# Performance work log

Measured on AMD Instinct MI355X. Metric: run time of the kernel, lower is better.

## Reference

```python
import jax, jax.numpy as jnp
import numpy as np

N_NODES = 50000
N_EDGES = 800000
IN_F = 128
OUT_F = 64
ALPHA = 0.2  # LeakyReLU negative slope


def setup_inputs() -> dict:
    key = jax.random.key(0)
    k_h, k_e, k_w, k_b, k_a = jax.random.split(key, 5)
    h = jax.random.normal(k_h, (N_NODES, IN_F), dtype=jnp.float32)
    adj = jax.random.randint(k_e, (2, N_EDGES), 0, N_NODES, dtype=jnp.int64)
    # Linear(in_features, out_features): weight [out, in], bias [out]
    W_w = jax.random.normal(k_w, (OUT_F, IN_F), dtype=jnp.float32) * (1.0 / np.sqrt(IN_F))
    W_b = jax.random.normal(k_b, (OUT_F,), dtype=jnp.float32) * 0.01
    a = jax.random.normal(k_a, (1, 2 * OUT_F), dtype=jnp.float32) * (1.0 / np.sqrt(2 * OUT_F))
    return {"h": h, "adj": adj, "W_w": W_w, "W_b": W_b, "a": a}


def reference(h, adj, W_w, W_b, a):
    N = h.shape[0]
    F_out = W_w.shape[0]
    inv_sqrt_f = 1.0 / float(np.sqrt(F_out))

    data = h @ W_w.T + W_b                      # [N, F_out]
    src, dst = adj[0], adj[1]

    # a @ [data[src] || data[dst]]^T  == (data @ a_src)[src] + (data @ a_dst)[dst]
    a_src, a_dst = a[0, :F_out], a[0, F_out:]
    score = (data @ a_src)[src] + (data @ a_dst)[dst]       # [E]
    edge_e = jnp.exp(jax.nn.leaky_relu(score, ALPHA) * inv_sqrt_f)

    # sparse rowsum over source rows (duplicate edges sum, matching COO semantics)
    rowsum = jax.ops.segment_sum(edge_e, src, num_segments=N)  # [N]
    row_zero = rowsum == 0.0
    rowsum = jnp.where(row_zero, 1.0, rowsum)

    # sparse mm: sum_e edge_e * data[dst] into row src; zero rows get a unit self-loop
    h_prime = jax.ops.segment_sum(edge_e[:, None] * data[dst], src, num_segments=N)
    h_prime = h_prime + row_zero[:, None].astype(data.dtype) * data
    return h_prime / rowsum[:, None]
```

## Files before the change

kernel.cpp:

```cpp
#include <hip/hip_runtime.h>
#include <math.h>

#define IN_F 128
#define OUT_F 64
#define ALPHA 0.2f
#define INV_SQRT_F 0.125f
#define CAP 64
#define BINSH 7
#define BINSZ 128
#define CAPB 4096
#define HS 136

typedef _Float16 h8  __attribute__((ext_vector_type(8)));
typedef float    f4  __attribute__((ext_vector_type(4)));

__device__ __forceinline__ float edge_w(float sc) {
    float lr = sc > 0.f ? sc : ALPHA * sc;
    return __expf(lr * INV_SQRT_F);
}

__device__ __forceinline__ h8 cvt8(float4 a, float4 b) {
    h8 r;
    r[0] = (_Float16)a.x; r[1] = (_Float16)a.y;
    r[2] = (_Float16)a.z; r[3] = (_Float16)a.w;
    r[4] = (_Float16)b.x; r[5] = (_Float16)b.y;
    r[6] = (_Float16)b.z; r[7] = (_Float16)b.w;
    return r;
}

__global__ __launch_bounds__(256, 4) void k_p1(
    const float* __restrict__ h, const float* __restrict__ W,
    const float* __restrict__ b, const float* __restrict__ a,
    const int* __restrict__ src, const int* __restrict__ dst,
    int* __restrict__ gcur, unsigned* __restrict__ pk,
    _Float16* __restrict__ data_h,
    float* __restrict__ s_src, float* __restrict__ s_dst,
    int n_nodes, int n_edges, int g_p1)
{
    __shared__ _Float16 wsh[OUT_F * HS];
    __shared__ int hist[512];
    __shared__ int off[512];
    const int tid = threadIdx.x;

    if ((int)blockIdx.x < g_p1) {
        const int nbins = (n_nodes + BINSZ - 1) >> BINSH;
        const int e0 = (int)blockIdx.x * 4096 + tid * 16;

        for (int i = tid; i < nbins; i += 256) hist[i] = 0;
        __syncthreads();

        int s[16], d[16];
        const bool full = (e0 + 16 <= n_edges);
        if (full) {
            #pragma unroll
            for (int c = 0; c < 4; ++c) {
                int4 s4 = *(const int4*)&src[e0 + c * 4];
                int4 d4 = *(const int4*)&dst[e0 + c * 4];
                s[c*4+0] = s4.x; s[c*4+1] = s4.y; s[c*4+2] = s4.z; s[c*4+3] = s4.w;
                d[c*4+0] = d4.x; d[c*4+1] = d4.y; d[c*4+2] = d4.z; d[c*4+3] = d4.w;
            }
            #pragma unroll
            for (int i = 0; i < 16; ++i)
                atomicAdd(&hist[s[i] >> BINSH], 1);
        } else {
            #pragma unroll
            for (int i = 0; i < 16; ++i) {
                int e = e0 + i;
                s[i] = (e < n_edges) ? src[e] : -1;
                d[i] = (e < n_edges) ? dst[e] : 0;
                if (s[i] >= 0) atomicAdd(&hist[s[i] >> BINSH], 1);
            }
        }
        __syncthreads();

        for (int i = tid; i < nbins; i += 256) {
            int c = hist[i];
            off[i] = (c > 0) ? atomicAdd(&gcur[i], c) : 0;
            hist[i] = 0;
        }
        __syncthreads();

        #pragma unroll
        for (int i = 0; i < 16; ++i) {
            if (s[i] < 0) continue;
            int bin = s[i] >> BINSH;
            int r = atomicAdd(&hist[bin], 1);
            int p = off[bin] + r;
            if (p < CAPB)
                pk[(size_t)bin * CAPB + p] =
                    ((unsigned)(s[i] & (BINSZ - 1)) << 16) | (unsigned)d[i];
        }
        return;
    }

    const int node0 = ((int)blockIdx.x - g_p1) * 64;

    const int wv  = tid >> 6;
    const int lane = tid & 63;
    const int q   = lane >> 4;
    const int col = lane & 15;
    const int r0  = wv * 16;

    const int arow = min(node0 + r0 + col, n_nodes - 1);
    const float* __restrict__ hrow = h + (size_t)arow * IN_F;

    float4 ha[4], hb[4];
    #pragma unroll
    for (int kk = 0; kk < 4; ++kk) {
        const int ko = kk * 32 + q * 8;
        ha[kk] = *(const float4*)&hrow[ko];
        hb[kk] = *(const float4*)&hrow[ko + 4];
    }
    float bb[4], as_[4], ad_[4];
    #pragma unroll
    for (int ct = 0; ct < 4; ++ct) {
        bb[ct]  = b[ct * 16 + col];
        as_[ct] = a[ct * 16 + col];
        ad_[ct] = a[OUT_F + ct * 16 + col];
    }

    for (int i = tid * 8; i < OUT_F * IN_F; i += 2048) {
        int f = i >> 7, k = i & 127;
        float4 va = *(const float4*)&W[i];
        float4 vb = *(const float4*)&W[i + 4];
        *(h8*)&wsh[f * HS + k] = cvt8(va, vb);
    }
    __syncthreads();

    f4 acc[4] = {{0.f,0.f,0.f,0.f},{0.f,0.f,0.f,0.f},
                 {0.f,0.f,0.f,0.f},{0.f,0.f,0.f,0.f}};
    #pragma unroll
    for (int kk = 0; kk < 4; ++kk) {
        const int ko = kk * 32 + q * 8;
        h8 av = cvt8(ha[kk], hb[kk]);
        #pragma unroll
        for (int ct = 0; ct < 4; ++ct) {
            h8 bv = *(const h8*)&wsh[(ct * 16 + col) * HS + ko];
            acc[ct] = __builtin_amdgcn_mfma_f32_16x16x32_f16(av, bv, acc[ct], 0, 0, 0);
        }
    }

    #pragma unroll
    for (int reg = 0; reg < 4; ++reg) {
        int n = node0 + r0 + q * 4 + reg;
        float vv[4], ps = 0.f, pd = 0.f;
        #pragma unroll
        for (int ct = 0; ct < 4; ++ct) {
            float v = acc[ct][reg] + bb[ct];
            vv[ct] = v;
            ps = fmaf(v, as_[ct], ps);
            pd = fmaf(v, ad_[ct], pd);
        }
        #pragma unroll
        for (int m = 1; m <= 8; m <<= 1) {
            ps += __shfl_xor(ps, m, 64);
            pd += __shfl_xor(pd, m, 64);
        }
        if (n < n_nodes) {
            size_t base = (size_t)n * OUT_F + col;
            #pragma unroll
            for (int ct = 0; ct < 4; ++ct)
                data_h[base + ct * 16] = (_Float16)vv[ct];
            if (col == 0) { s_src[n] = ps; s_dst[n] = pd; }
        }
    }
}

__global__ __launch_bounds__(512) void k_bin(
    const unsigned* __restrict__ pk, const int* __restrict__ gcur,
    const float* __restrict__ s_src, const float* __restrict__ s_dst,
    const _Float16* __restrict__ data_h, float* __restrict__ out, int n_nodes)
{
    __shared__ uint2 edl[64 * CAP];
    __shared__ int   lcnt[64];
    __shared__ float ssl[64];
    const int bin  = (int)blockIdx.x >> 1;
    const int half = (int)blockIdx.x & 1;
    const int tid  = threadIdx.x;
    const int nbase = bin * BINSZ + half * 64;

    if (tid < 64) {
        lcnt[tid] = 0;
        int n = nbase + tid;
        ssl[tid] = (n < n_nodes) ? s_src[n] : 0.f;
    }
    __syncthreads();

    const int ecnt = min(gcur[bin], CAPB);
    for (int i = tid; i < ecnt; i += 512) {
        unsigned v = pk[(size_t)bin * CAPB + i];
        int sl = (int)(v >> 16);
        if ((sl >> 6) == half) {
            int s63 = sl & 63;
            int d = (int)(v & 0xffffu);
            float w = edge_w(ssl[s63] + s_dst[d]);
            int r = atomicAdd(&lcnt[s63], 1);
            if (r < CAP) {
                uint2 e; e.x = (unsigned)d; e.y = __float_as_uint(w);
                edl[s63 * CAP + r] = e;
            }
        }
    }
    __syncthreads();

    const int wv = tid >> 6, lane = tid & 63;
    const int g  = lane >> 3;
    const int fl = lane & 7;

    #pragma unroll 1
    for (int ni = 0; ni < 8; ++ni) {
        const int nl = wv * 8 + ni;
        const int n = nbase + nl;
        if (n >= n_nodes) break;
        const int cn = min(lcnt[nl], CAP);
        const int bbase = nl * CAP;

        float ac[8] = {0.f,0.f,0.f,0.f,0.f,0.f,0.f,0.f};
        float rs = 0.f;
        int t = 0;
        for (; t + 16 <= cn; t += 16) {
            uint2 e0 = edl[bbase + t + g];
            uint2 e1 = edl[bbase + t + 8 + g];
            float w0 = __uint_as_float(e0.y);
            float w1 = __uint_as_float(e1.y);
            h8 x0 = *(const h8*)&data_h[(size_t)e0.x * OUT_F + 8 * fl];
            h8 x1 = *(const h8*)&data_h[(size_t)e1.x * OUT_F + 8 * fl];
            #pragma unroll
            for (int i = 0; i < 8; ++i) ac[i] = fmaf(w0, (float)x0[i], ac[i]);
            #pragma unroll
            for (int i = 0; i < 8; ++i) ac[i] = fmaf(w1, (float)x1[i], ac[i]);
            rs += w0 + w1;
        }
        for (; t + 8 <= cn; t += 8) {
            uint2 e0 = edl[bbase + t + g];
            float w0 = __uint_as_float(e0.y);
            h8 x0 = *(const h8*)&data_h[(size_t)e0.x * OUT_F + 8 * fl];
            #pragma unroll
            for (int i = 0; i < 8; ++i) ac[i] = fmaf(w0, (float)x0[i], ac[i]);
            rs += w0;
        }
        const int rem = cn - t;
        if (g < rem) {
            uint2 e0 = edl[bbase + t + g];
            float w0 = __uint_as_float(e0.y);
            h8 x0 = *(const h8*)&data_h[(size_t)e0.x * OUT_F + 8 * fl];
            #pragma unroll
            for (int i = 0; i < 8; ++i) ac[i] = fmaf(w0, (float)x0[i], ac[i]);
            rs += w0;
        }
        #pragma unroll
        for (int m = 8; m <= 32; m <<= 1) {
            #pragma unroll
            for (int i = 0; i < 8; ++i) ac[i] += __shfl_xor(ac[i], m, 64);
            rs += __shfl_xor(rs, m, 64);
        }

        if (g == 0) {
            size_t o = (size_t)n * OUT_F + 8 * fl;
            f4 r0, r1;
            if (rs == 0.f) {
                h8 xv = *(const h8*)&data_h[o];
                r0[0] = (float)xv[0]; r0[1] = (float)xv[1];
                r0[2] = (float)xv[2]; r0[3] = (float)xv[3];
                r1[0] = (float)xv[4]; r1[1] = (float)xv[5];
                r1[2] = (float)xv[6]; r1[3] = (float)xv[7];
            } else {
                float inv = 1.f / rs;
                r0[0] = ac[0] * inv; r0[1] = ac[1] * inv;
                r0[2] = ac[2] * inv; r0[3] = ac[3] * inv;
                r1[0] = ac[4] * inv; r1[1] = ac[5] * inv;
                r1[2] = ac[6] * inv; r1[3] = ac[7] * inv;
            }
            __builtin_nontemporal_store(r0, (f4*)&out[o]);
            __builtin_nontemporal_store(r1, (f4*)&out[o + 4]);
        }
    }
}

extern "C" void kernel_launch(void* const* d_in, const int* in_sizes, int n_in,
                              void* d_out, int out_size, void* d_ws, size_t ws_size,
                              hipStream_t stream)
{
    const float* h   = (const float*)d_in[0];
    const int*   adj = (const int*)  d_in[1];
    const float* W   = (const float*)d_in[2];
    const float* b   = (const float*)d_in[3];
    const float* a   = (const float*)d_in[4];
    float* out = (float*)d_out;

    const int n_nodes = in_sizes[0] / IN_F;
    const int n_edges = in_sizes[1] / 2;
    const int* src = adj;
    const int* dst = adj + n_edges;
    const int nbins = (n_nodes + BINSZ - 1) >> BINSH;

    char* p = (char*)d_ws;
    _Float16*       data_h = (_Float16*)p;       p += (size_t)n_nodes * OUT_F * 2;
    unsigned*       pk     = (unsigned*)p;       p += (size_t)nbins * CAPB * 4;
    float*          s_src  = (float*)p;          p += (size_t)n_nodes * 4;
    float*          s_dst  = (float*)p;          p += (size_t)n_nodes * 4;
    int*            gcur   = (int*)p;            p += (size_t)nbins * 4;

    (void)hipMemsetAsync(gcur, 0, (size_t)nbins * sizeof(int), stream);

    const int g_p1  = (n_edges + 4095) / 4096;
    const int g_lin = (n_nodes + 63) / 64;
    k_p1<<<g_p1 + g_lin, 256, 0, stream>>>(
        h, W, b, a, src, dst, gcur, pk, data_h, s_src, s_dst,
        n_nodes, n_edges, g_p1);

    k_bin<<<nbins * 2, 512, 0, stream>>>(
        pk, gcur, s_src, s_dst, data_h, out, n_nodes);
}
```

Measured before the change: 125.8 us.

## Assign one node per 8-lane group and rotate LDS edge slots

The aggregation phase drops the per-node loop where a whole wave split each node's edges across 8 lane groups and then reduced them with shuffles. Now each 8-lane group handles one node alone, walking its edges serially with 4-way unrolled gathers, so the cross-group shuffle reduction disappears. Edge slots in LDS are rotated by node index so that groups reading different nodes at the same step hit different banks. This trades fewer shuffles and less idle time on short lists for load imbalance between groups whose nodes have different degrees, and for a serial dependency chain per group.

```diff
diff --git a/kernel.cpp b/kernel.cpp
--- a/kernel.cpp
+++ b/kernel.cpp
@@ -197,7 +197,7 @@
             int r = atomicAdd(&lcnt[s63], 1);
             if (r < CAP) {
                 uint2 e; e.x = (unsigned)d; e.y = __float_as_uint(w);
-                edl[s63 * CAP + r] = e;
+                edl[s63 * CAP + ((r + 2 * (s63 & 7)) & (CAP - 1))] = e;
             }
         }
     }
@@ -206,74 +206,65 @@
     const int wv = tid >> 6, lane = tid & 63;
     const int g  = lane >> 3;
     const int fl = lane & 7;
-
-    #pragma unroll 1
-    for (int ni = 0; ni < 8; ++ni) {
-        const int nl = wv * 8 + ni;
-        const int n = nbase + nl;
-        if (n >= n_nodes) break;
-        const int cn = min(lcnt[nl], CAP);
-        const int bbase = nl * CAP;
-
-        float ac[8] = {0.f,0.f,0.f,0.f,0.f,0.f,0.f,0.f};
-        float rs = 0.f;
-        int t = 0;
-        for (; t + 16 <= cn; t += 16) {
-            uint2 e0 = edl[bbase + t + g];
-            uint2 e1 = edl[bbase + t + 8 + g];
-            float w0 = __uint_as_float(e0.y);
-            float w1 = __uint_as_float(e1.y);
-            h8 x0 = *(const h8*)&data_h[(size_t)e0.x * OUT_F + 8 * fl];
-            h8 x1 = *(const h8*)&data_h[(size_t)e1.x * OUT_F + 8 * fl];
-            #pragma unroll
-            for (int i = 0; i < 8; ++i) ac[i] = fmaf(w0, (float)x0[i], ac[i]);
-            #pragma unroll
-            for (int i = 0; i < 8; ++i) ac[i] = fmaf(w1, (float)x1[i], ac[i]);
-            rs += w0 + w1;
-        }
-        for (; t + 8 <= cn; t += 8) {
-            uint2 e0 = edl[bbase + t + g];
-            float w0 = __uint_as_float(e0.y);
-            h8 x0 = *(const h8*)&data_h[(size_t)e0.x * OUT_F + 8 * fl];
-            #pragma unroll
-            for (int i = 0; i < 8; ++i) ac[i] = fmaf(w0, (float)x0[i], ac[i]);
-            rs += w0;
-        }
-        const int rem = cn - t;
-        if (g < rem) {
-            uint2 e0 = edl[bbase + t + g];
-            float w0 = __uint_as_float(e0.y);
-            h8 x0 = *(const h8*)&data_h[(size_t)e0.x * OUT_F + 8 * fl];
-            #pragma unroll
-            for (int i = 0; i < 8; ++i) ac[i] = fmaf(w0, (float)x0[i], ac[i]);
-            rs += w0;
-        }
-        #pragma unroll
-        for (int m = 8; m <= 32; m <<= 1) {
-            #pragma unroll
-            for (int i = 0; i < 8; ++i) ac[i] += __shfl_xor(ac[i], m, 64);
-            rs += __shfl_xor(rs, m, 64);
-        }
-
-        if (g == 0) {
-            size_t o = (size_t)n * OUT_F + 8 * fl;
-            f4 r0, r1;
-            if (rs == 0.f) {
-                h8 xv = *(const h8*)&data_h[o];
-                r0[0] = (float)xv[0]; r0[1] = (float)xv[1];
-                r0[2] = (float)xv[2]; r0[3] = (float)xv[3];
-                r1[0] = (float)xv[4]; r1[1] = (float)xv[5];
-                r1[2] = (float)xv[6]; r1[3] = (float)xv[7];
-            } else {
-                float inv = 1.f / rs;
-                r0[0] = ac[0] * inv; r0[1] = ac[1] * inv;
-                r0[2] = ac[2] * inv; r0[3] = ac[3] * inv;
-                r1[0] = ac[4] * inv; r1[1] = ac[5] * inv;
-                r1[2] = ac[6] * inv; r1[3] = ac[7] * inv;
-            }
-            __builtin_nontemporal_store(r0, (f4*)&out[o]);
-            __builtin_nontemporal_store(r1, (f4*)&out[o + 4]);
-        }
+    const int nl = wv * 8 + g;
+    const int n  = nbase + nl;
+    const int rot = 2 * (nl & 7);
+    const int cn = (n < n_nodes) ? min(lcnt[nl], CAP) : 0;
+    const int bbase = nl * CAP;
+
+    float ac[8] = {0.f,0.f,0.f,0.f,0.f,0.f,0.f,0.f};
+    float rs = 0.f;
+    int t = 0;
+    for (; t + 4 <= cn; t += 4) {
+        uint2 e0 = edl[bbase + ((t + 0 + rot) & (CAP - 1))];
+        uint2 e1 = edl[bbase + ((t + 1 + rot) & (CAP - 1))];
+        uint2 e2 = edl[bbase + ((t + 2 + rot) & (CAP - 1))];
+        uint2 e3 = edl[bbase + ((t + 3 + rot) & (CAP - 1))];
+        h8 x0 = *(const h8*)&data_h[(size_t)e0.x * OUT_F + 8 * fl];
+        h8 x1 = *(const h8*)&data_h[(size_t)e1.x * OUT_F + 8 * fl];
+        h8 x2 = *(const h8*)&data_h[(size_t)e2.x * OUT_F + 8 * fl];
+        h8 x3 = *(const h8*)&data_h[(size_t)e3.x * OUT_F + 8 * fl];
+        float w0 = __uint_as_float(e0.y);
+        float w1 = __uint_as_float(e1.y);
+        float w2 = __uint_as_float(e2.y);
+        float w3 = __uint_as_float(e3.y);
+        #pragma unroll
+        for (int i = 0; i < 8; ++i) ac[i] = fmaf(w0, (float)x0[i], ac[i]);
+        #pragma unroll
+        for (int i = 0; i < 8; ++i) ac[i] = fmaf(w1, (float)x1[i], ac[i]);
+        #pragma unroll
+        for (int i = 0; i < 8; ++i) ac[i] = fmaf(w2, (float)x2[i], ac[i]);
+        #pragma unroll
+        for (int i = 0; i < 8; ++i) ac[i] = fmaf(w3, (float)x3[i], ac[i]);
+        rs += (w0 + w1) + (w2 + w3);
+    }
+    for (; t < cn; ++t) {
+        uint2 e0 = edl[bbase + ((t + rot) & (CAP - 1))];
+        float w0 = __uint_as_float(e0.y);
+        h8 x0 = *(const h8*)&data_h[(size_t)e0.x * OUT_F + 8 * fl];
+        #pragma unroll
+        for (int i = 0; i < 8; ++i) ac[i] = fmaf(w0, (float)x0[i], ac[i]);
+        rs += w0;
+    }
+
+    if (n < n_nodes) {
+        size_t o = (size_t)n * OUT_F + 8 * fl;
+        f4 r0, r1;
+        if (rs == 0.f) {
+            h8 xv = *(const h8*)&data_h[o];
+            r0[0] = (float)xv[0]; r0[1] = (float)xv[1];
+            r0[2] = (float)xv[2]; r0[3] = (float)xv[3];
+            r1[0] = (float)xv[4]; r1[1] = (float)xv[5];
+            r1[2] = (float)xv[6]; r1[3] = (float)xv[7];
+        } else {
+            float inv = 1.f / rs;
+            r0[0] = ac[0] * inv; r0[1] = ac[1] * inv;
+            r0[2] = ac[2] * inv; r0[3] = ac[3] * inv;
+            r1[0] = ac[4] * inv; r1[1] = ac[5] * inv;
+            r1[2] = ac[6] * inv; r1[3] = ac[7] * inv;
+        }
+        __builtin_nontemporal_store(r0, (f4*)&out[o]);
+        __builtin_nontemporal_store(r1, (f4*)&out[o + 4]);
     }
 }
 
```

Result: faster. 112.4 us (-10.7%).
